# Kernel tuning notes

Hardware: AMD Instinct MI355X
Metric: run time of the kernel (lower is better)

## Reference

```python
import jax, jax.numpy as jnp
import numpy as np

N, S, EMB, H = 4, 2048, 512, 8
D = EMB // H  # 64


def setup_inputs() -> dict:
    key = jax.random.key(0)
    ks = jax.random.split(key, 10)
    sc = 0.02
    return {
        "x": jax.random.normal(ks[0], (N, S, EMB), dtype=jnp.float32),
        "Wq": jax.random.normal(ks[1], (D, D), dtype=jnp.float32) * sc,
        "bq": jax.random.normal(ks[2], (D,), dtype=jnp.float32) * sc,
        "Wk": jax.random.normal(ks[3], (D, D), dtype=jnp.float32) * sc,
        "bk": jax.random.normal(ks[4], (D,), dtype=jnp.float32) * sc,
        "Wv": jax.random.normal(ks[5], (D, D), dtype=jnp.float32) * sc,
        "bv": jax.random.normal(ks[6], (D,), dtype=jnp.float32) * sc,
        "E": jax.random.normal(ks[7], (1, S, D), dtype=jnp.float32),
        "Wo": jax.random.normal(ks[8], (EMB, EMB), dtype=jnp.float32) * sc,
        "bo": jax.random.normal(ks[9], (EMB,), dtype=jnp.float32) * sc,
    }


def reference(x, Wq, bq, Wk, bk, Wv, bv, E, Wo, bo):
    n, s, emb = x.shape
    h, d = H, D
    xh = x.reshape(n, s, h, d)
    # per-head Linear projections (torch Linear: y = x @ W.T + b)
    q = xh @ Wq.T + bq  # [n,s,h,d]
    k = xh @ Wk.T + bk
    v = xh @ Wv.T + bv

    # QE = queries.transpose(1,2) @ E.transpose(1,2) -> [n,h,s,s]
    QE = jnp.einsum('nqhd,sd->nhqs', q, E[0])
    # _mask_positions: zero where triu(ones(S,S),1) flipped along columns == 1
    triu1 = jnp.triu(jnp.ones((s, s), dtype=bool), 1)
    QE = jnp.where(triu1[:, ::-1], 0.0, QE)
    # _skew: pad last dim on the left, reinterpret (s, s+1) as (s+1, s), drop first row
    padded = jnp.pad(QE, ((0, 0), (0, 0), (0, 0), (1, 0)))  # [n,h,s,s+1]
    Smat = padded.reshape(n, h, s + 1, s)[:, :, 1:, :]  # [n,h,s,s]

    qk = jnp.einsum('nqhd,nkhd->nhqk', q, k)
    # faithful to source: fill where mask==0 (lower triangle incl. diag) with -1e20
    qk = jnp.where(triu1, qk, jnp.float32(-1e20))
    attention = jax.nn.softmax(qk / (emb ** 0.5), axis=3) + Smat

    z = jnp.einsum('nhql,nlhd->nqhd', attention, v).reshape(n, s, h * d)
    return z @ Wo.T + bo


if __name__ == "__main__":
    out = reference(**setup_inputs())
    print(out.shape, out.dtype)
```

## Files before the change

### kernel.cpp

```cpp
#include <hip/hip_runtime.h>
#include <hip/hip_bf16.h>

#define S_LEN 2048
#define EMB   512
#define NH    8
#define DH    64
#define NB    4

typedef float f32x4  __attribute__((ext_vector_type(4)));
typedef short short8 __attribute__((ext_vector_type(8)));

__device__ __forceinline__ unsigned short f2bf_rn(float f) {
    return __builtin_bit_cast(unsigned short, __float2bfloat16(f));
}

__device__ __forceinline__ f32x4 mfma16(short8 a, short8 b, f32x4 c) {
    return __builtin_amdgcn_mfma_f32_16x16x32_bf16(a, b, c, 0, 0, 0);
}

__device__ __forceinline__ short8 frag_read(const unsigned short* lds, int row, int oct)
{
    const char* src = (const char*)lds + row * 128 + ((oct * 16) ^ ((row & 7) << 4));
    return *reinterpret_cast<const short8*>(src);
}

__device__ __forceinline__ int pinv(int k) {
    return (k & 32) + ((k >> 2) & 3) * 8 + (k & 3) + ((k & 16) >> 2);
}

__device__ __forceinline__ void stage_tile_f32(const float* __restrict__ g,
                                               int gstride, unsigned short* lds, int tid)
{
    #pragma unroll
    for (int c = tid; c < 512; c += 256) {
        const int r = c >> 3, s = c & 7;
        const float4* src = (const float4*)(g + (size_t)r * gstride + s * 8);
        const float4 a = src[0], b = src[1];
        short8 f;
        f[0] = (short)f2bf_rn(a.x); f[1] = (short)f2bf_rn(a.y);
        f[2] = (short)f2bf_rn(a.z); f[3] = (short)f2bf_rn(a.w);
        f[4] = (short)f2bf_rn(b.x); f[5] = (short)f2bf_rn(b.y);
        f[6] = (short)f2bf_rn(b.z); f[7] = (short)f2bf_rn(b.w);
        char* dst = (char*)lds + r * 128 + ((s * 16) ^ ((r & 7) << 4));
        *reinterpret_cast<short8*>(dst) = f;
    }
}

__device__ __forceinline__ void softmax_pack(const f32x4 C[4], bool diag, int ws, int og,
                                             int rowg, float& dsum, short8& pa0, short8& pa1)
{
    constexpr float SM_SCALE = 0.04419417382415922f;
    float rs[4];
    unsigned short pw[16];
    if (!diag) {
        #pragma unroll
        for (int t = 0; t < 4; ++t) {
            float a = 0.f;
            #pragma unroll
            for (int r = 0; r < 4; ++r) {
                const float wv = __expf(C[t][r] * SM_SCALE);
                a += wv;
                pw[t * 4 + r] = f2bf_rn(wv);
            }
            rs[t] = a;
        }
    } else {
        #pragma unroll
        for (int t = 0; t < 4; ++t) {
            float a = 0.f;
            #pragma unroll
            for (int r = 0; r < 4; ++r) {
                const bool keep = (t > ws) || (t == ws && (og * 4 + r) > rowg);
                const float wv = keep ? __expf(C[t][r] * SM_SCALE) : 0.f;
                a += wv;
                pw[t * 4 + r] = f2bf_rn(wv);
            }
            rs[t] = a;
        }
    }
    dsum += (rs[0] + rs[1]) + (rs[2] + rs[3]);
    #pragma unroll
    for (int i = 0; i < 8; ++i) { pa0[i] = (short)pw[i]; pa1[i] = (short)pw[8 + i]; }
}

__global__ __launch_bounds__(256) void qkv_mfma(
    const float* __restrict__ x,
    const float* __restrict__ Wq, const float* __restrict__ bq,
    const float* __restrict__ Wk, const float* __restrict__ bk,
    const float* __restrict__ Wv, const float* __restrict__ bv,
    unsigned short* __restrict__ qg, unsigned short* __restrict__ kg,
    unsigned short* __restrict__ vg)
{
    __shared__ unsigned short w_lds[3][64 * 64];

    const int tid  = threadIdx.x;
    const int lane = tid & 63;
    const int w    = tid >> 6;
    const int rowg = lane & 15;
    const int og   = lane >> 4;

    stage_tile_f32(Wq, 64, w_lds[0], tid);
    stage_tile_f32(Wk, 64, w_lds[1], tid);
    stage_tile_f32(Wv, 64, w_lds[2], tid);

    float bias[3][4];
    #pragma unroll
    for (int t = 0; t < 4; ++t) {
        bias[0][t] = bq[16 * t + rowg];
        bias[1][t] = bk[16 * t + rowg];
        bias[2][t] = bv[16 * t + rowg];
    }

    const int m0 = blockIdx.x * 64 + 16 * w;
    const float* xr = x + (size_t)(m0 + rowg) * 64;
    const float4 a0 = *(const float4*)(xr + og * 8);
    const float4 a1 = *(const float4*)(xr + og * 8 + 4);
    const float4 a2 = *(const float4*)(xr + 32 + og * 8);
    const float4 a3 = *(const float4*)(xr + 32 + og * 8 + 4);
    short8 af0, af1;
    af0[0] = (short)f2bf_rn(a0.x); af0[1] = (short)f2bf_rn(a0.y);
    af0[2] = (short)f2bf_rn(a0.z); af0[3] = (short)f2bf_rn(a0.w);
    af0[4] = (short)f2bf_rn(a1.x); af0[5] = (short)f2bf_rn(a1.y);
    af0[6] = (short)f2bf_rn(a1.z); af0[7] = (short)f2bf_rn(a1.w);
    af1[0] = (short)f2bf_rn(a2.x); af1[1] = (short)f2bf_rn(a2.y);
    af1[2] = (short)f2bf_rn(a2.z); af1[3] = (short)f2bf_rn(a2.w);
    af1[4] = (short)f2bf_rn(a3.x); af1[5] = (short)f2bf_rn(a3.y);
    af1[6] = (short)f2bf_rn(a3.z); af1[7] = (short)f2bf_rn(a3.w);

    __syncthreads();

    f32x4 acc[3][4];
    #pragma unroll
    for (int m = 0; m < 3; ++m)
        #pragma unroll
        for (int t = 0; t < 4; ++t) {
            const float b = bias[m][t];
            acc[m][t] = (f32x4){b, b, b, b};
        }

    #pragma unroll
    for (int m = 0; m < 3; ++m)
        #pragma unroll
        for (int t = 0; t < 4; ++t) {
            acc[m][t] = mfma16(af0, frag_read(w_lds[m], 16 * t + rowg, og),     acc[m][t]);
            acc[m][t] = mfma16(af1, frag_read(w_lds[m], 16 * t + rowg, og + 4), acc[m][t]);
        }

    unsigned short* outp[3] = {qg, kg, vg};
    #pragma unroll
    for (int m = 0; m < 3; ++m)
        #pragma unroll
        for (int r = 0; r < 4; ++r) {
            const int mr = (blockIdx.x * 64 + 16 * w) + og * 4 + r;
            const int tk = mr >> 3, h = mr & 7;
            const int n = tk >> 11, s = tk & 2047;
            const size_t rowb = (((size_t)(n * NH + h)) * S_LEN + s) * 64;
            #pragma unroll
            for (int t = 0; t < 4; ++t)
                outp[m][rowb + 16 * t + rowg] = f2bf_rn(acc[m][t][r]);
        }
}

__global__ __launch_bounds__(256) void transpose_v(
    const unsigned short* __restrict__ v, unsigned short* __restrict__ vt)
{
    __shared__ unsigned short t_lds[64][72];
    const int bid = blockIdx.x;
    const int st = bid % (S_LEN / 64);
    const int nh = bid / (S_LEN / 64);
    const unsigned short* vp = v + ((size_t)nh * S_LEN + st * 64) * DH;
    unsigned short* vtp = vt + (size_t)nh * DH * S_LEN + st * 64;
    const int tid = threadIdx.x;
    #pragma unroll
    for (int c = tid; c < 512; c += 256) {
        const int r = c >> 3, s = c & 7;
        short8 xv = *reinterpret_cast<const short8*>(vp + r * DH + s * 8);
        #pragma unroll
        for (int i = 0; i < 8; ++i) t_lds[s * 8 + i][r] = (unsigned short)xv[i];
    }
    __syncthreads();
    #pragma unroll
    for (int c = tid; c < 512; c += 256) {
        const int d = c >> 3, sc = c & 7;
        const int cb = ((sc & 4) << 3) + (sc & 3) * 4;
        short8 y;
        #pragma unroll
        for (int i = 0; i < 8; ++i)
            y[i] = (short)t_lds[d][cb + (i & 3) + ((i & 4) << 2)];
        *reinterpret_cast<short8*>(vtp + (size_t)d * S_LEN + sc * 8) = y;
    }
}

__global__ __launch_bounds__(256) void prep_e(
    const float* __restrict__ E, unsigned short* __restrict__ eb)
{
    const int i = blockIdx.x * 256 + threadIdx.x;
    if (i >= S_LEN * DH) return;
    const int dlt = i >> 6, d = i & 63;
    eb[i] = f2bf_rn(E[(size_t)(S_LEN - 1 - dlt) * DH + d]);
}

__global__ __launch_bounds__(256) void attn_mfma(
    const unsigned short* __restrict__ qg,
    const unsigned short* __restrict__ kg,
    const unsigned short* __restrict__ vtg,
    const unsigned short* __restrict__ eg,
    unsigned short* __restrict__ z)
{
    __shared__ __align__(16) unsigned short smem[20480];

    constexpr float UNI = 1.0f / 2048.0f;

    const int nqt = S_LEN / 64;
    const int bid = blockIdx.x;
    const int qt  = (nqt - 1) - (bid >> 5);
    const int nh  = bid & 31;
    const int q0  = qt * 64;
    const size_t base = (size_t)nh * S_LEN * DH;
    const unsigned short* qp = qg + base;
    const unsigned short* kp = kg + base;
    const unsigned short* vp = vtg + base;

    const int tid  = threadIdx.x;
    const int lane = tid & 63;
    const int w    = tid >> 6;
    const int rowg = lane & 15;
    const int og   = lane >> 4;

    const int r0 = tid >> 3,  s0 = tid & 7;
    const int r1 = r0 + 32;
    const int ldsoff0 = r0 * 128 + ((s0 * 16) ^ ((r0 & 7) << 4));
    const int ldsoff1 = r1 * 128 + ((s0 * 16) ^ ((r1 & 7) << 4));
    const int ksrc0 = r0 * 64 + s0 * 8,    ksrc1 = r1 * 64 + s0 * 8;
    const int vsrc0 = r0 * S_LEN + s0 * 8, vsrc1 = r1 * S_LEN + s0 * 8;

    short8 kr0, kr1, vr0, vr1;

    short8 qa0, qa1;
    {
        const unsigned short* qr = qp + (size_t)(q0 + 16 * w + rowg) * DH + og * 8;
        qa0 = *reinterpret_cast<const short8*>(qr);
        qa1 = *reinterpret_cast<const short8*>(qr + 32);
    }

    const f32x4 zero4 = {0.f, 0.f, 0.f, 0.f};
    f32x4 accS[4], accR[4];
    #pragma unroll
    for (int t = 0; t < 4; ++t) { accS[t] = zero4; accR[t] = zero4; }
    float dsum = 0.f;

    const int T = (S_LEN - q0) >> 6;
    kr0 = *(const short8*)(kp + (size_t)q0 * 64 + ksrc0);
    kr1 = *(const short8*)(kp + (size_t)q0 * 64 + ksrc1);
    vr0 = *(const short8*)(vp + q0 + vsrc0);
    vr1 = *(const short8*)(vp + q0 + vsrc1);
    *(short8*)((char*)smem + ldsoff0) = kr0;
    *(short8*)((char*)smem + ldsoff1) = kr1;
    *(short8*)((char*)(smem + 8192) + ldsoff0) = vr0;
    *(short8*)((char*)(smem + 8192) + ldsoff1) = vr1;
    __syncthreads();

    short8 pa0, pa1;
    for (int ti = 0; ti < T; ++ti) {
        const bool pf = (ti + 1 < T);
        if (pf) {
            const unsigned short* kb = kp + (size_t)(q0 + (ti + 1) * 64) * 64;
            const unsigned short* vb = vp + (q0 + (ti + 1) * 64);
            kr0 = *(const short8*)(kb + ksrc0);
            kr1 = *(const short8*)(kb + ksrc1);
            vr0 = *(const short8*)(vb + vsrc0);
            vr1 = *(const short8*)(vb + vsrc1);
        }
        const unsigned short* klds = smem + (ti & 1) * 4096;

        __builtin_amdgcn_s_setprio(1);
        f32x4 C[4];
        #pragma unroll
        for (int t = 0; t < 4; ++t) {
            const short8 kf0 = frag_read(klds, 16 * t + rowg, og);
            const short8 kf1 = frag_read(klds, 16 * t + rowg, og + 4);
            C[t] = mfma16(kf1, qa1, mfma16(kf0, qa0, zero4));
        }
        if (ti > 0) {
            const unsigned short* vprev = smem + 8192 + ((ti + 2) % 3) * 4096;
            #pragma unroll
            for (int tt = 0; tt < 4; ++tt) {
                const short8 vf0 = frag_read(vprev, 16 * tt + rowg, og);
                const short8 vf1 = frag_read(vprev, 16 * tt + rowg, og + 4);
                accS[tt] = mfma16(pa1, vf1, mfma16(pa0, vf0, accS[tt]));
            }
        }
        __builtin_amdgcn_s_setprio(0);

        if (pf) {
            unsigned short* kn = smem + ((ti + 1) & 1) * 4096;
            unsigned short* vn = smem + 8192 + ((ti + 1) % 3) * 4096;
            *(short8*)((char*)kn + ldsoff0) = kr0;
            *(short8*)((char*)kn + ldsoff1) = kr1;
            *(short8*)((char*)vn + ldsoff0) = vr0;
            *(short8*)((char*)vn + ldsoff1) = vr1;
        }
        softmax_pack(C, ti == 0, w, og, rowg, dsum, pa0, pa1);
        __syncthreads();
    }
    {
        const unsigned short* vprev = smem + 8192 + ((T + 2) % 3) * 4096;
        __builtin_amdgcn_s_setprio(1);
        #pragma unroll
        for (int tt = 0; tt < 4; ++tt) {
            const short8 vf0 = frag_read(vprev, 16 * tt + rowg, og);
            const short8 vf1 = frag_read(vprev, 16 * tt + rowg, og + 4);
            accS[tt] = mfma16(pa1, vf1, mfma16(pa0, vf0, accS[tt]));
        }
        __builtin_amdgcn_s_setprio(0);
    }
    __syncthreads();

    unsigned short* const ebuf = smem + 16384;
    const int jmax = q0 >> 6;

    kr0 = *(const short8*)(eg + ksrc0);
    kr1 = *(const short8*)(eg + ksrc1);
    vr0 = *(const short8*)(vp + q0 + vsrc0);
    vr1 = *(const short8*)(vp + q0 + vsrc1);
    {
        const short8 z8 = {0, 0, 0, 0, 0, 0, 0, 0};
        #pragma unroll
        for (int c2 = 0; c2 < 2; ++c2) {
            const int cc = lane + 64 * c2;
            const int r = 16 * w + (cc >> 3), sc = cc & 7;
            *reinterpret_cast<short8*>((char*)smem + r * 128 + sc * 16) = z8;
        }
    }
    *(short8*)((char*)ebuf + ldsoff0) = kr0;
    *(short8*)((char*)ebuf + ldsoff1) = kr1;
    *(short8*)((char*)(smem + 8192) + ldsoff0) = vr0;
    *(short8*)((char*)(smem + 8192) + ldsoff1) = vr1;
    __syncthreads();

    for (int j = 0; j <= jmax; ++j) {
        const bool pf = (j < jmax);
        if (pf) {
            const unsigned short* ebn = eg + (size_t)(j + 1) * 4096;
            const unsigned short* vbn = vp + (q0 - 64 * (j + 1));
            kr0 = *(const short8*)(ebn + ksrc0);
            kr1 = *(const short8*)(ebn + ksrc1);
            vr0 = *(const short8*)(vbn + vsrc0);
            vr1 = *(const short8*)(vbn + vsrc1);
        }
        const unsigned short* vlds = smem + 8192 + (j & 1) * 4096;

        __builtin_amdgcn_s_setprio(1);
        f32x4 G[4];
        #pragma unroll
        for (int t = 0; t < 4; ++t)
            G[t] = mfma16(qa1, frag_read(ebuf, 16 * t + rowg, og + 4),
                   mfma16(qa0, frag_read(ebuf, 16 * t + rowg, og), zero4));
        __builtin_amdgcn_s_setprio(0);

        unsigned short* pc = smem + (j & 1) * 4096;
        unsigned short* pn = smem + ((j + 1) & 1) * 4096;
        #pragma unroll
        for (int t = 0; t < 4; ++t) {
            const int c = 16 * t + rowg;
            #pragma unroll
            for (int r = 0; r < 4; ++r) {
                const int qq = 16 * w + og * 4 + r;
                float val = G[t][r];
                if (q0 + qq == S_LEN - 1) val += UNI;
                const unsigned short bv = f2bf_rn(val);
                const int swz = (qq & 7) << 4;
                if (c <= qq) {
                    const int p = pinv(qq - c);
                    *(unsigned short*)((char*)pc + qq * 128 + ((p * 2) ^ swz)) = bv;
                } else if (pf) {
                    const int p = pinv(qq - c + 64);
                    *(unsigned short*)((char*)pn + qq * 128 + ((p * 2) ^ swz)) = bv;
                }
            }
        }

        const short8 pb0 = frag_read(pc, 16 * w + rowg, og);
        const short8 pb1 = frag_read(pc, 16 * w + rowg, og + 4);
        __builtin_amdgcn_s_setprio(1);
        #pragma unroll
        for (int tt = 0; tt < 4; ++tt) {
            const short8 vf0 = frag_read(vlds, 16 * tt + rowg, og);
            const short8 vf1 = frag_read(vlds, 16 * tt + rowg, og + 4);
            accR[tt] = mfma16(pb1, vf1, mfma16(pb0, vf0, accR[tt]));
        }
        __builtin_amdgcn_s_setprio(0);

        __syncthreads();
        if (pf) {
            unsigned short* vn = smem + 8192 + ((j + 1) & 1) * 4096;
            *(short8*)((char*)ebuf + ldsoff0) = kr0;
            *(short8*)((char*)ebuf + ldsoff1) = kr1;
            *(short8*)((char*)vn + ldsoff0) = vr0;
            *(short8*)((char*)vn + ldsoff1) = vr1;
            __syncthreads();
        }
    }

    dsum += __shfl_xor(dsum, 16);
    dsum += __shfl_xor(dsum, 32);

    const int n = nh >> 3, h = nh & 7;
    const int qrow0 = q0 + 16 * w + og * 4;
    #pragma unroll
    for (int r = 0; r < 4; ++r) {
        const int qrow = qrow0 + r;
        const float dn = __shfl(dsum, og * 4 + r);
        const float inv = (qrow == S_LEN - 1) ? 0.f : 1.f / dn;
        #pragma unroll
        for (int t = 0; t < 4; ++t) {
            const float zv = accS[t][r] * inv + accR[t][r];
            z[((size_t)n * S_LEN + qrow) * EMB + h * DH + 16 * t + rowg] = f2bf_rn(zv);
        }
    }
}

__global__ __launch_bounds__(256) void outproj_mfma(
    const unsigned short* __restrict__ z,
    const float* __restrict__ Wo, const float* __restrict__ bo,
    float* __restrict__ out)
{
    __shared__ unsigned short wo_lds[64 * 64];

    const int tid  = threadIdx.x;
    const int lane = tid & 63;
    const int w    = tid >> 6;
    const int rowg = lane & 15;
    const int og   = lane >> 4;

    const int nob = EMB / 64;
    const int mb = blockIdx.x / nob;
    const int ob = blockIdx.x % nob;
    const int m0 = mb * 64 + 16 * w;
    const int o0 = ob * 64;

    f32x4 acc[4];
    #pragma unroll
    for (int t = 0; t < 4; ++t) {
        const float b = bo[o0 + 16 * t + rowg];
        acc[t] = (f32x4){b, b, b, b};
    }

    for (int k0 = 0; k0 < EMB; k0 += 64) {
        __syncthreads();
        stage_tile_f32(Wo + (size_t)o0 * EMB + k0, EMB, wo_lds, tid);
        __syncthreads();
        const unsigned short* zr = z + (size_t)(m0 + rowg) * EMB + k0;
        const short8 af0 = *reinterpret_cast<const short8*>(zr + og * 8);
        const short8 af1 = *reinterpret_cast<const short8*>(zr + 32 + og * 8);
        #pragma unroll
        for (int t = 0; t < 4; ++t) {
            acc[t] = mfma16(af0, frag_read(wo_lds, 16 * t + rowg, og),     acc[t]);
            acc[t] = mfma16(af1, frag_read(wo_lds, 16 * t + rowg, og + 4), acc[t]);
        }
    }

    #pragma unroll
    for (int r = 0; r < 4; ++r) {
        const size_t rowb = (size_t)(m0 + og * 4 + r) * EMB + o0;
        #pragma unroll
        for (int t = 0; t < 4; ++t)
            out[rowb + 16 * t + rowg] = acc[t][r];
    }
}

extern "C" void kernel_launch(void* const* d_in, const int* in_sizes, int n_in,
                              void* d_out, int out_size, void* d_ws, size_t ws_size,
                              hipStream_t stream) {
    const float* x  = (const float*)d_in[0];
    const float* Wq = (const float*)d_in[1];
    const float* bq = (const float*)d_in[2];
    const float* Wk = (const float*)d_in[3];
    const float* bk = (const float*)d_in[4];
    const float* Wv = (const float*)d_in[5];
    const float* bv = (const float*)d_in[6];
    const float* E  = (const float*)d_in[7];
    const float* Wo = (const float*)d_in[8];
    const float* bo = (const float*)d_in[9];
    float* out = (float*)d_out;

    const size_t per = (size_t)NB * NH * S_LEN * DH;
    unsigned short* qb  = (unsigned short*)d_ws;
    unsigned short* kb  = qb  + per;
    unsigned short* vb  = kb  + per;
    unsigned short* vtb = vb  + per;
    unsigned short* eb  = vtb + per;
    unsigned short* zb  = eb + (size_t)S_LEN * DH;

    qkv_mfma<<<(NB * S_LEN * NH) / 64, 256, 0, stream>>>(x, Wq, bq, Wk, bk, Wv, bv,
                                                         qb, kb, vb);
    transpose_v<<<NB * NH * (S_LEN / 64), 256, 0, stream>>>(vb, vtb);
    prep_e<<<(S_LEN * DH + 255) / 256, 256, 0, stream>>>(E, eb);
    attn_mfma<<<NB * NH * (S_LEN / 64), 256, 0, stream>>>(qb, kb, vtb, eb, zb);
    outproj_mfma<<<(NB * S_LEN / 64) * (EMB / 64), 256, 0, stream>>>(zb, Wo, bo, out);
}
```

Baseline: 102.5 us.

## Pre-convert weights to bf16, double-buffer Wo tiles, use exp2 in softmax

```diff
diff --git a/kernel.cpp b/kernel.cpp
--- a/kernel.cpp
+++ b/kernel.cpp
@@ -28,28 +28,22 @@
     return (k & 32) + ((k >> 2) & 3) * 8 + (k & 3) + ((k & 16) >> 2);
 }
 
-__device__ __forceinline__ void stage_tile_f32(const float* __restrict__ g,
-                                               int gstride, unsigned short* lds, int tid)
+__device__ __forceinline__ void stage_tile_bf16(const unsigned short* __restrict__ g,
+                                                int gstride, unsigned short* lds, int tid)
 {
     #pragma unroll
     for (int c = tid; c < 512; c += 256) {
         const int r = c >> 3, s = c & 7;
-        const float4* src = (const float4*)(g + (size_t)r * gstride + s * 8);
-        const float4 a = src[0], b = src[1];
-        short8 f;
-        f[0] = (short)f2bf_rn(a.x); f[1] = (short)f2bf_rn(a.y);
-        f[2] = (short)f2bf_rn(a.z); f[3] = (short)f2bf_rn(a.w);
-        f[4] = (short)f2bf_rn(b.x); f[5] = (short)f2bf_rn(b.y);
-        f[6] = (short)f2bf_rn(b.z); f[7] = (short)f2bf_rn(b.w);
+        short8 v = *reinterpret_cast<const short8*>(g + (size_t)r * gstride + s * 8);
         char* dst = (char*)lds + r * 128 + ((s * 16) ^ ((r & 7) << 4));
-        *reinterpret_cast<short8*>(dst) = f;
+        *reinterpret_cast<short8*>(dst) = v;
     }
 }
 
 __device__ __forceinline__ void softmax_pack(const f32x4 C[4], bool diag, int ws, int og,
                                              int rowg, float& dsum, short8& pa0, short8& pa1)
 {
-    constexpr float SM_SCALE = 0.04419417382415922f;
+    constexpr float SM_SC2 = 0.06375861597263857f;
     float rs[4];
     unsigned short pw[16];
     if (!diag) {
@@ -58,7 +52,7 @@
             float a = 0.f;
             #pragma unroll
             for (int r = 0; r < 4; ++r) {
-                const float wv = __expf(C[t][r] * SM_SCALE);
+                const float wv = __builtin_exp2f(C[t][r] * SM_SC2);
                 a += wv;
                 pw[t * 4 + r] = f2bf_rn(wv);
             }
@@ -71,7 +65,7 @@
             #pragma unroll
             for (int r = 0; r < 4; ++r) {
                 const bool keep = (t > ws) || (t == ws && (og * 4 + r) > rowg);
-                const float wv = keep ? __expf(C[t][r] * SM_SCALE) : 0.f;
+                const float wv = keep ? __builtin_exp2f(C[t][r] * SM_SC2) : 0.f;
                 a += wv;
                 pw[t * 4 + r] = f2bf_rn(wv);
             }
@@ -83,11 +77,26 @@
     for (int i = 0; i < 8; ++i) { pa0[i] = (short)pw[i]; pa1[i] = (short)pw[8 + i]; }
 }
 
+__global__ __launch_bounds__(256) void prep_w(
+    const float* __restrict__ Wq, const float* __restrict__ Wk,
+    const float* __restrict__ Wv, const float* __restrict__ Wo,
+    unsigned short* __restrict__ wq, unsigned short* __restrict__ wk,
+    unsigned short* __restrict__ wv, unsigned short* __restrict__ wo)
+{
+    const int i = blockIdx.x * 256 + threadIdx.x;
+    if (i < 4096) {
+        wq[i] = f2bf_rn(Wq[i]);
+        wk[i] = f2bf_rn(Wk[i]);
+        wv[i] = f2bf_rn(Wv[i]);
+    }
+    if (i < EMB * EMB) wo[i] = f2bf_rn(Wo[i]);
+}
+
 __global__ __launch_bounds__(256) void qkv_mfma(
     const float* __restrict__ x,
-    const float* __restrict__ Wq, const float* __restrict__ bq,
-    const float* __restrict__ Wk, const float* __restrict__ bk,
-    const float* __restrict__ Wv, const float* __restrict__ bv,
+    const unsigned short* __restrict__ Wqb, const float* __restrict__ bq,
+    const unsigned short* __restrict__ Wkb, const float* __restrict__ bk,
+    const unsigned short* __restrict__ Wvb, const float* __restrict__ bv,
     unsigned short* __restrict__ qg, unsigned short* __restrict__ kg,
     unsigned short* __restrict__ vg)
 {
@@ -99,9 +108,9 @@
     const int rowg = lane & 15;
     const int og   = lane >> 4;
 
-    stage_tile_f32(Wq, 64, w_lds[0], tid);
-    stage_tile_f32(Wk, 64, w_lds[1], tid);
-    stage_tile_f32(Wv, 64, w_lds[2], tid);
+    stage_tile_bf16(Wqb, 64, w_lds[0], tid);
+    stage_tile_bf16(Wkb, 64, w_lds[1], tid);
+    stage_tile_bf16(Wvb, 64, w_lds[2], tid);
 
     float bias[3][4];
     #pragma unroll
@@ -422,10 +431,10 @@
 
 __global__ __launch_bounds__(256) void outproj_mfma(
     const unsigned short* __restrict__ z,
-    const float* __restrict__ Wo, const float* __restrict__ bo,
+    const unsigned short* __restrict__ Wob, const float* __restrict__ bo,
     float* __restrict__ out)
 {
-    __shared__ unsigned short wo_lds[64 * 64];
+    __shared__ unsigned short wo_lds[2][64 * 64];
 
     const int tid  = threadIdx.x;
     const int lane = tid & 63;
@@ -439,6 +448,13 @@
     const int m0 = mb * 64 + 16 * w;
     const int o0 = ob * 64;
 
+    const int r0 = tid >> 3,  s0 = tid & 7;
+    const int r1 = r0 + 32;
+    const int ldsoff0 = r0 * 128 + ((s0 * 16) ^ ((r0 & 7) << 4));
+    const int ldsoff1 = r1 * 128 + ((s0 * 16) ^ ((r1 & 7) << 4));
+    const int wsrc0 = r0 * EMB + s0 * 8, wsrc1 = r1 * EMB + s0 * 8;
+    const unsigned short* wbase = Wob + (size_t)o0 * EMB;
+
     f32x4 acc[4];
     #pragma unroll
     for (int t = 0; t < 4; ++t) {
@@ -446,18 +462,33 @@
         acc[t] = (f32x4){b, b, b, b};
     }
 
-    for (int k0 = 0; k0 < EMB; k0 += 64) {
-        __syncthreads();
-        stage_tile_f32(Wo + (size_t)o0 * EMB + k0, EMB, wo_lds, tid);
-        __syncthreads();
-        const unsigned short* zr = z + (size_t)(m0 + rowg) * EMB + k0;
+    short8 wr0 = *(const short8*)(wbase + wsrc0);
+    short8 wr1 = *(const short8*)(wbase + wsrc1);
+    *(short8*)((char*)wo_lds[0] + ldsoff0) = wr0;
+    *(short8*)((char*)wo_lds[0] + ldsoff1) = wr1;
+    __syncthreads();
+
+    int cur = 0;
+    for (int kt = 0; kt < 8; ++kt) {
+        const bool pf = (kt < 7);
+        if (pf) {
+            wr0 = *(const short8*)(wbase + (kt + 1) * 64 + wsrc0);
+            wr1 = *(const short8*)(wbase + (kt + 1) * 64 + wsrc1);
+        }
+        const unsigned short* zr = z + (size_t)(m0 + rowg) * EMB + kt * 64;
         const short8 af0 = *reinterpret_cast<const short8*>(zr + og * 8);
         const short8 af1 = *reinterpret_cast<const short8*>(zr + 32 + og * 8);
         #pragma unroll
         for (int t = 0; t < 4; ++t) {
-            acc[t] = mfma16(af0, frag_read(wo_lds, 16 * t + rowg, og),     acc[t]);
-            acc[t] = mfma16(af1, frag_read(wo_lds, 16 * t + rowg, og + 4), acc[t]);
-        }
+            acc[t] = mfma16(af0, frag_read(wo_lds[cur], 16 * t + rowg, og),     acc[t]);
+            acc[t] = mfma16(af1, frag_read(wo_lds[cur], 16 * t + rowg, og + 4), acc[t]);
+        }
+        if (pf) {
+            *(short8*)((char*)wo_lds[cur ^ 1] + ldsoff0) = wr0;
+            *(short8*)((char*)wo_lds[cur ^ 1] + ldsoff1) = wr1;
+        }
+        __syncthreads();
+        cur ^= 1;
     }
 
     #pragma unroll
@@ -491,11 +522,17 @@
     unsigned short* vtb = vb  + per;
     unsigned short* eb  = vtb + per;
     unsigned short* zb  = eb + (size_t)S_LEN * DH;
-
-    qkv_mfma<<<(NB * S_LEN * NH) / 64, 256, 0, stream>>>(x, Wq, bq, Wk, bk, Wv, bv,
+    unsigned short* wqb = zb + per * 2;
+    unsigned short* wkb = wqb + 4096;
+    unsigned short* wvb = wkb + 4096;
+    unsigned short* wob = wvb + 4096;
+
+    prep_w<<<(EMB * EMB + 255) / 256, 256, 0, stream>>>(Wq, Wk, Wv, Wo,
+                                                        wqb, wkb, wvb, wob);
+    qkv_mfma<<<(NB * S_LEN * NH) / 64, 256, 0, stream>>>(x, wqb, bq, wkb, bk, wvb, bv,
                                                          qb, kb, vb);
     transpose_v<<<NB * NH * (S_LEN / 64), 256, 0, stream>>>(vb, vtb);
     prep_e<<<(S_LEN * DH + 255) / 256, 256, 0, stream>>>(E, eb);
     attn_mfma<<<NB * NH * (S_LEN / 64), 256, 0, stream>>>(qb, kb, vtb, eb, zb);
-    outproj_mfma<<<(NB * S_LEN / 64) * (EMB / 64), 256, 0, stream>>>(zb, Wo, bo, out);
-}
+    outproj_mfma<<<(NB * S_LEN / 64) * (EMB / 64), 256, 0, stream>>>(zb, wob, bo, out);
+}
```

Result: slower. 109.4 us (+6.7%).
